# Performance work log

Measured on AMD Instinct MI355X. Metric: run time of the kernel, lower is better.

The kernel has to match this reference:

```python
import jax, jax.numpy as jnp
import numpy as np

D = 768      # input_dim
O = 768      # output_dim
E = 8        # num_experts
H = 10 * D   # expert hidden dim (fixed by module: input_dim * 10)
N = 4096     # tokens


def setup_inputs() -> dict:
    key = jax.random.key(0)
    ks = jax.random.split(key, 7)
    s = lambda fan_in: 1.0 / np.sqrt(fan_in)
    x  = jax.random.normal(ks[0], (N, D), dtype=jnp.float32)
    Wg = jax.random.uniform(ks[1], (D, E), jnp.float32, -s(D), s(D))
    bg = jax.random.uniform(ks[2], (E,),   jnp.float32, -s(D), s(D))
    W1 = jax.random.uniform(ks[3], (E, D, H), jnp.float32, -s(D), s(D))
    b1 = jax.random.uniform(ks[4], (E, H),    jnp.float32, -s(D), s(D))
    W2 = jax.random.uniform(ks[5], (E, H, O), jnp.float32, -s(H), s(H))
    b2 = jax.random.uniform(ks[6], (E, O),    jnp.float32, -s(H), s(H))
    return {"x": x, "Wg": Wg, "bg": bg, "W1": W1, "b1": b1, "W2": W2, "b2": b2}


def reference(x, Wg, bg, W1, b1, W2, b2):
    # gating: softmax over experts, keep only top-1 prob (rest zeroed)
    gate_probs = jax.nn.softmax(x @ Wg + bg, axis=1)          # [N, E]
    top_vals, top_idx = jax.lax.top_k(gate_probs, 1)           # [N, 1]
    gate_masked = jnp.zeros_like(gate_probs).at[
        jnp.arange(x.shape[0]), top_idx[:, 0]].set(top_vals[:, 0])
    # dense all-experts MLP (module computes every expert for every token)
    h = jax.nn.relu(jnp.einsum('nd,edh->neh', x, W1) + b1)     # [N, E, H]
    expert_out = jnp.einsum('neh,eho->neo', h, W2) + b2        # [N, E, O]
    # bmm combine: [N,1,E] @ [N,E,O] -> [N,O]
    return jnp.einsum('ne,neo->no', gate_masked, expert_out)
```

## Files before the change

### kernel.cpp

```cpp
#include <hip/hip_runtime.h>
#include <hip/hip_bf16.h>
#include <stdint.h>

#define N_TOK 4096
#define DIM   768
#define NE    8
#define HDIM  7680
#define ODIM  768
#define G1GRID 2816
#define G2GRID 1344

typedef __bf16 bf16x8 __attribute__((ext_vector_type(8)));
typedef float f32x4 __attribute__((ext_vector_type(4)));

__device__ __forceinline__ unsigned short f2bf(float f) {
    union { float f; unsigned u; } v; v.f = f;
    return (unsigned short)((v.u + 0x7fffu + ((v.u >> 16) & 1u)) >> 16);
}

__device__ __forceinline__ unsigned cvt_pk_bf16(float lo, float hi) {
    unsigned r;
    asm("v_cvt_pk_bf16_f32 %0, %1, %2" : "=v"(r) : "v"(lo), "v"(hi));
    return r;
}

__device__ __forceinline__ void gload_lds16(const unsigned short* g, unsigned short* l) {
    __builtin_amdgcn_global_load_lds(
        (const __attribute__((address_space(1))) unsigned int*)g,
        (__attribute__((address_space(3))) unsigned int*)l, 16, 0, 0);
}

__global__ void moe_gating(const float* __restrict__ x, const float* __restrict__ Wg,
                           const float* __restrict__ bg, int* __restrict__ cnt,
                           int* __restrict__ top_e, int* __restrict__ rnk,
                           float* __restrict__ top_p) {
    const int wid  = threadIdx.x >> 6;
    const int lane = threadIdx.x & 63;
    const int t = blockIdx.x * 4 + wid;
    double p[NE];
#pragma unroll
    for (int j = 0; j < NE; ++j) p[j] = 0.0;
    const float* xr  = x  + (size_t)t * DIM + lane * 12;
    const float* wr0 = Wg + lane * 12 * NE;
#pragma unroll
    for (int i = 0; i < 12; ++i) {
        double xv = (double)xr[i];
#pragma unroll
        for (int j = 0; j < NE; ++j) p[j] += xv * (double)wr0[i * NE + j];
    }
#pragma unroll
    for (int off = 32; off >= 1; off >>= 1)
#pragma unroll
        for (int j = 0; j < NE; ++j) p[j] += __shfl_xor(p[j], off, 64);
    if (lane == 0) {
        double l[NE];
#pragma unroll
        for (int j = 0; j < NE; ++j) l[j] = p[j] + (double)bg[j];
        int be = 0; double bl = l[0];
#pragma unroll
        for (int j = 1; j < NE; ++j) if (l[j] > bl) { bl = l[j]; be = j; }
        double s = 0.0;
#pragma unroll
        for (int j = 0; j < NE; ++j) s += exp(l[j] - bl);
        int rk = atomicAdd(&cnt[be], 1);
        top_e[t] = be; rnk[t] = rk; top_p[t] = (float)(1.0 / s);
    }
}

__global__ void moe_init(int* cnt) { if (threadIdx.x < NE) cnt[threadIdx.x] = 0; }

__global__ void moe_scan(const int* __restrict__ cnt, int* __restrict__ offs,
                         int* __restrict__ mc, int* __restrict__ g1s,
                         int* __restrict__ g2s) {
    __shared__ int smc[NE];
    int tid = threadIdx.x;
    if (tid == 0) { int s = 0; for (int e = 0; e < NE; ++e) { offs[e] = s; s += cnt[e]; } }
    if (tid < NE) { smc[tid] = (cnt[tid] + 127) >> 7; mc[tid] = smc[tid]; }
    __syncthreads();
    if (tid < 8) {
        int s = 0;
        for (int j = 0; j < 60; ++j) { int p = tid + 8 * j; g1s[p] = s; s += smc[p / 60]; }
        int s2 = 0;
        for (int j = 0; j < 6; ++j)  { int p = tid + 8 * j; g2s[p] = s2; s2 += 4 * smc[p / 6]; }
    }
}

__global__ void moe_fill(const int* __restrict__ mc, const int* __restrict__ g1s,
                         const int* __restrict__ g2s, int* __restrict__ tbl1,
                         int* __restrict__ tbl2) {
    int gid = blockIdx.x * 256 + threadIdx.x;
    if (gid < G1GRID) {
        int c = gid & 7, slot = gid >> 3;
        int sel = c;
        for (int j = 0; j < 60; ++j) { int p = c + 8 * j; if (g1s[p] <= slot) sel = p; else break; }
        int e = sel / 60, n0 = sel % 60;
        int mt = slot - g1s[sel];
        tbl1[gid] = (mt < mc[e]) ? ((e << 14) | (mt << 8) | (n0 << 2)) : -1;
    } else if (gid < G1GRID + G2GRID) {
        int gg = gid - G1GRID;
        int c = gg & 7, slot = gg >> 3;
        int sel = c;
        for (int j = 0; j < 6; ++j) { int p = c + 8 * j; if (g2s[p] <= slot) sel = p; else break; }
        int e = sel / 6, n0 = sel % 6;
        int mem = slot - g2s[sel];
        int mcE = mc[e];
        int ks = mem / mcE, mt = mem - ks * mcE;
        tbl2[gg] = (mem < 4 * mcE) ? ((e << 14) | (mt << 8) | (n0 << 2) | ks) : -1;
    }
}

__global__ void moe_mkperm(const int* __restrict__ top_e, const int* __restrict__ rnk,
                           const float* __restrict__ top_p, const int* __restrict__ offs,
                           int* __restrict__ perm, float* __restrict__ gate_s) {
    int t = blockIdx.x * 256 + threadIdx.x;
    int e = top_e[t];
    int slot = offs[e] + rnk[t];
    perm[slot] = t;
    gate_s[slot] = top_p[t];
}

__global__ void moe_gather(const float* __restrict__ x, const int* __restrict__ perm,
                           unsigned short* __restrict__ Xg) {
    int slot = blockIdx.x;
    int t = perm[slot];
    const float* src = x + (size_t)t * DIM;
    unsigned short* dst = Xg + (size_t)slot * DIM;
    for (int i = threadIdx.x; i < DIM; i += 256) dst[i] = f2bf(src[i]);
}

__global__ void moe_initout(const int* __restrict__ top_e, const float* __restrict__ top_p,
                            const float* __restrict__ b2, float* __restrict__ out) {
    int t = blockIdx.x;
    int e = top_e[t];
    float gv = top_p[t];
    const float* b = b2 + (size_t)e * ODIM;
    float* o = out + (size_t)t * ODIM;
    for (int i = threadIdx.x; i < ODIM; i += 256) o[i] = gv * b[i];
}

template<int LAYER>
__global__ __launch_bounds__(256, 3) void moe_gemm(
    const unsigned short* __restrict__ A, const float* __restrict__ B,
    const float* __restrict__ bias, const int* __restrict__ cnt,
    const int* __restrict__ offs, const int* __restrict__ perm,
    const float* __restrict__ gate_s, const int* __restrict__ tbl,
    unsigned short* __restrict__ H, float* __restrict__ out) {

    constexpr int NT    = (LAYER == 1) ? HDIM : ODIM;
    constexpr int AST   = (LAYER == 1) ? DIM  : HDIM;
    constexpr int KFULL = (LAYER == 1) ? DIM  : HDIM;
    constexpr int KBLK  = (LAYER == 1) ? DIM  : HDIM / 4;
    constexpr int NITER = KBLK / 32;

    const int code = tbl[blockIdx.x];
    if (code < 0) return;
    const int e  = code >> 14;
    const int mt = (code >> 8) & 63;
    const int n0 = ((code >> 2) & 63) * 128;
    const int ks = code & 3;
    const int ne = cnt[e];
    const int base = offs[e];
    const int mlim = ne - mt * 128;
    const int kbase = ks * KBLK;

    __shared__ __align__(16) unsigned short As[3][4096];
    __shared__ __align__(16) unsigned short Bs[2][4096];

    const int tid = threadIdx.x;
    const int lane = tid & 63, w = tid >> 6;
    const int wr = w >> 1, wc = w & 1;
    const int g = lane >> 4, r = lane & 15;

    const int rl0 = 2 * w * 16 + r;
    const int rl1 = rl0 + 16;
    const int cr0 = rl0 < mlim ? rl0 : mlim - 1;
    const int cr1 = rl1 < mlim ? rl1 : mlim - 1;
    const unsigned short* aS0 = A + (size_t)(base + mt * 128 + cr0) * AST + kbase + g * 8;
    const unsigned short* aS1 = A + (size_t)(base + mt * 128 + cr1) * AST + kbase + g * 8;
    const int aD0 = (2 * w) * 512;
    const int aD1 = aD0 + 512;

    const int bn = tid & 127;
    const int kh = tid >> 7;
    const float* bS = B + (size_t)e * KFULL * NT + (size_t)(kbase + kh * 16) * NT + n0 + bn;
    const int bD = (bn >> 4) * 512 + (kh * 2) * 128 + (bn & 15) * 8;

    f32x4 acc[4][4] = {};
    float bvA[16], bvB[16];

    unsigned short* A0 = &As[0][0];
    unsigned short* A1 = &As[1][0];
    unsigned short* A2 = &As[2][0];

#define LOADB(dst_, t_)                                                        \
    do { const float* bp_ = bS + (size_t)((t_) * 32) * NT;                     \
        _Pragma("unroll")                                                      \
        for (int i_ = 0; i_ < 16; ++i_) dst_[i_] = bp_[(size_t)i_ * NT];       \
    } while (0)

#define DMA_A(t_, abase_)                                                      \
    do { gload_lds16(aS0 + (t_) * 32, (abase_) + aD0);                         \
         gload_lds16(aS1 + (t_) * 32, (abase_) + aD1); } while (0)

#define COMMITB(src_, buf_)                                                    \
    do { uint4 q0_, q1_;                                                       \
        q0_.x = cvt_pk_bf16(src_[0],  src_[1]);  q0_.y = cvt_pk_bf16(src_[2],  src_[3]);  \
        q0_.z = cvt_pk_bf16(src_[4],  src_[5]);  q0_.w = cvt_pk_bf16(src_[6],  src_[7]);  \
        q1_.x = cvt_pk_bf16(src_[8],  src_[9]);  q1_.y = cvt_pk_bf16(src_[10], src_[11]); \
        q1_.z = cvt_pk_bf16(src_[12], src_[13]); q1_.w = cvt_pk_bf16(src_[14], src_[15]); \
        *(uint4*)&Bs[buf_][bD]       = q0_;                                    \
        *(uint4*)&Bs[buf_][bD + 128] = q1_;                                    \
    } while (0)

#define PHASE_END                                                              \
    do { asm volatile("s_waitcnt lgkmcnt(0)" ::: "memory");                    \
         __builtin_amdgcn_s_barrier();                                         \
         __builtin_amdgcn_sched_barrier(0); } while (0)

#define BODY(t_, cur_, ARD_, ADMA_, LDst_, CMsrc_, MODE_)                      \
    do {                                                                       \
        bf16x8 af_[4], bf_[4];                                                 \
        _Pragma("unroll")                                                      \
        for (int m_ = 0; m_ < 4; ++m_)                                         \
            af_[m_] = *(const bf16x8*)((ARD_) + (wr * 4 + m_) * 512 + lane * 8); \
        _Pragma("unroll")                                                      \
        for (int n_ = 0; n_ < 4; ++n_)                                         \
            bf_[n_] = *(const bf16x8*)&Bs[cur_][(wc * 4 + n_) * 512 + lane * 8]; \
        if (MODE_ == 2) DMA_A((t_) + 2, ADMA_);                                \
        if (MODE_ == 2) LOADB(LDst_, (t_) + 2);                                \
        _Pragma("unroll")                                                      \
        for (int n_ = 0; n_ < 4; ++n_)                                         \
            _Pragma("unroll")                                                  \
            for (int m_ = 0; m_ < 4; ++m_)                                     \
                acc[m_][n_] = __builtin_amdgcn_mfma_f32_16x16x32_bf16(         \
                    af_[m_], bf_[n_], acc[m_][n_], 0, 0, 0);                   \
        if (MODE_ >= 1) { COMMITB(CMsrc_, (cur_) ^ 1); PHASE_END; }            \
    } while (0)

    DMA_A(0, A0);
    LOADB(bvA, 0);
    DMA_A(1, A1);
    LOADB(bvB, 1);
    COMMITB(bvA, 0);
    PHASE_END;

#pragma unroll 1
    for (int t = 0; t + 4 <= NITER; t += 2) {
        BODY(t,     0, A0, A2, bvA, bvB, 2);
        BODY(t + 1, 1, A1, A0, bvB, bvA, 2);
        unsigned short* tr_ = A2; A2 = A1; A1 = A0; A0 = tr_;
    }
    BODY(NITER - 2, 0, A0, A2, bvA, bvB, 1);
    BODY(NITER - 1, 1, A1, A2, bvB, bvA, 0);

#undef BODY
#undef PHASE_END
#undef COMMITB
#undef DMA_A
#undef LOADB

#pragma unroll
    for (int m = 0; m < 4; ++m) {
#pragma unroll
        for (int j = 0; j < 4; ++j) {
            int lrow = mt * 128 + wr * 64 + m * 16 + g * 4 + j;
            if (lrow < ne) {
                int slot = base + lrow;
#pragma unroll
                for (int n = 0; n < 4; ++n) {
                    int col = n0 + wc * 64 + n * 16 + r;
                    if constexpr (LAYER == 1) {
                        float v = acc[m][n][j] + bias[(size_t)e * NT + col];
                        v = fmaxf(v, 0.0f);
                        H[(size_t)slot * HDIM + col] = f2bf(v);
                    } else {
                        atomicAdd(&out[(size_t)perm[slot] * ODIM + col],
                                  gate_s[slot] * acc[m][n][j]);
                    }
                }
            }
        }
    }
}

extern "C" void kernel_launch(void* const* d_in, const int* in_sizes, int n_in,
                              void* d_out, int out_size, void* d_ws, size_t ws_size,
                              hipStream_t stream) {
    const float* x  = (const float*)d_in[0];
    const float* Wg = (const float*)d_in[1];
    const float* bg = (const float*)d_in[2];
    const float* W1 = (const float*)d_in[3];
    const float* b1 = (const float*)d_in[4];
    const float* W2 = (const float*)d_in[5];
    const float* b2 = (const float*)d_in[6];
    float* out = (float*)d_out;

    char* ws = (char*)d_ws;
    int*   cnt    = (int*)(ws + 0);
    int*   offs   = (int*)(ws + 64);
    int*   mc     = (int*)(ws + 128);
    int*   g1s    = (int*)(ws + 256);
    int*   g2s    = (int*)(ws + 2304);
    int*   tbl1   = (int*)(ws + 3072);
    int*   tbl2   = (int*)(ws + 14336);
    int*   top_e  = (int*)(ws + 19712);
    int*   rnk    = (int*)(ws + 19712 + 16384);
    float* top_p  = (float*)(ws + 19712 + 2 * 16384);
    int*   perm   = (int*)(ws + 19712 + 3 * 16384);
    float* gate_s = (float*)(ws + 19712 + 4 * 16384);
    unsigned short* Xg = (unsigned short*)(ws + 101632);
    unsigned short* H  = (unsigned short*)(ws + 101632 + (size_t)N_TOK * DIM * 2);

    moe_init<<<1, 64, 0, stream>>>(cnt);
    moe_gating<<<N_TOK / 4, 256, 0, stream>>>(x, Wg, bg, cnt, top_e, rnk, top_p);
    moe_scan<<<1, 64, 0, stream>>>(cnt, offs, mc, g1s, g2s);
    moe_fill<<<(G1GRID + G2GRID + 255) / 256, 256, 0, stream>>>(mc, g1s, g2s, tbl1, tbl2);
    moe_mkperm<<<N_TOK / 256, 256, 0, stream>>>(top_e, rnk, top_p, offs, perm, gate_s);
    moe_gather<<<N_TOK, 256, 0, stream>>>(x, perm, Xg);
    moe_initout<<<N_TOK, 256, 0, stream>>>(top_e, top_p, b2, out);

    moe_gemm<1><<<G1GRID, 256, 0, stream>>>(Xg, W1, b1, cnt, offs, perm, gate_s, tbl1, H, out);
    moe_gemm<2><<<G2GRID, 256, 0, stream>>>(H, W2, b2, cnt, offs, perm, gate_s, tbl2, H, out);
}
```

Before: 369.0 us.

## Pre-transpose weights to bf16 and use 256-row, 512-thread GEMM tiles

Adds a transpose kernel that converts W1 and W2 from fp32 to bf16, K-major, on every call, so both operands can be streamed straight into LDS with global_load_lds. The grouped GEMM now uses 512-thread blocks with 256-row M tiles, a K step of 64 and a triple-buffered shared buffer. Tile count halves (smaller grid tables), and per-iteration register conversion of B is removed. In exchange, each call pays an extra pass that reads all weights in fp32 and writes them back in bf16, and occupancy drops to one block per CU.

New measurement: 459.1 us. 24.4% more time.

```diff
diff --git a/kernel.cpp b/kernel.cpp
--- a/kernel.cpp
+++ b/kernel.cpp
@@ -7,8 +7,8 @@
 #define NE    8
 #define HDIM  7680
 #define ODIM  768
-#define G1GRID 2816
-#define G2GRID 1344
+#define G1GRID 1536
+#define G2GRID 768
 
 typedef __bf16 bf16x8 __attribute__((ext_vector_type(8)));
 typedef float f32x4 __attribute__((ext_vector_type(4)));
@@ -16,12 +16,6 @@
 __device__ __forceinline__ unsigned short f2bf(float f) {
     union { float f; unsigned u; } v; v.f = f;
     return (unsigned short)((v.u + 0x7fffu + ((v.u >> 16) & 1u)) >> 16);
-}
-
-__device__ __forceinline__ unsigned cvt_pk_bf16(float lo, float hi) {
-    unsigned r;
-    asm("v_cvt_pk_bf16_f32 %0, %1, %2" : "=v"(r) : "v"(lo), "v"(hi));
-    return r;
 }
 
 __device__ __forceinline__ void gload_lds16(const unsigned short* g, unsigned short* l) {
@@ -75,7 +69,7 @@
     __shared__ int smc[NE];
     int tid = threadIdx.x;
     if (tid == 0) { int s = 0; for (int e = 0; e < NE; ++e) { offs[e] = s; s += cnt[e]; } }
-    if (tid < NE) { smc[tid] = (cnt[tid] + 127) >> 7; mc[tid] = smc[tid]; }
+    if (tid < NE) { smc[tid] = (cnt[tid] + 255) >> 8; mc[tid] = smc[tid]; }
     __syncthreads();
     if (tid < 8) {
         int s = 0;
@@ -138,9 +132,38 @@
     for (int i = threadIdx.x; i < ODIM; i += 256) o[i] = gv * b[i];
 }
 
+__global__ __launch_bounds__(256) void moe_wtrans(const float* __restrict__ in,
+                                                  unsigned short* __restrict__ outw,
+                                                  int K, int N) {
+    __shared__ __align__(16) unsigned short t[64][72];
+    const int tid = threadIdx.x;
+    const float* src = in + (size_t)blockIdx.z * K * N + (size_t)(blockIdx.y * 64) * N
+                          + blockIdx.x * 64;
+    unsigned short* dst = outw + (size_t)blockIdx.z * K * N + (size_t)(blockIdx.x * 64) * K
+                               + blockIdx.y * 64;
+    const int kr = tid >> 4;
+    const int nc = (tid & 15) * 4;
+#pragma unroll
+    for (int p = 0; p < 4; ++p) {
+        float4 v = *(const float4*)(src + (size_t)(p * 16 + kr) * N + nc);
+        t[nc + 0][p * 16 + kr] = f2bf(v.x);
+        t[nc + 1][p * 16 + kr] = f2bf(v.y);
+        t[nc + 2][p * 16 + kr] = f2bf(v.z);
+        t[nc + 3][p * 16 + kr] = f2bf(v.w);
+    }
+    __syncthreads();
+    const int nr = tid >> 3;
+    const int kc = (tid & 7) * 8;
+#pragma unroll
+    for (int p = 0; p < 2; ++p) {
+        uint4 q = *(const uint4*)&t[p * 32 + nr][kc];
+        *(uint4*)(dst + (size_t)(p * 32 + nr) * K + kc) = q;
+    }
+}
+
 template<int LAYER>
-__global__ __launch_bounds__(256, 3) void moe_gemm(
-    const unsigned short* __restrict__ A, const float* __restrict__ B,
+__global__ __launch_bounds__(512, 1) void moe_gemm8(
+    const unsigned short* __restrict__ A, const unsigned short* __restrict__ Wt,
     const float* __restrict__ bias, const int* __restrict__ cnt,
     const int* __restrict__ offs, const int* __restrict__ perm,
     const float* __restrict__ gate_s, const int* __restrict__ tbl,
@@ -150,7 +173,7 @@
     constexpr int AST   = (LAYER == 1) ? DIM  : HDIM;
     constexpr int KFULL = (LAYER == 1) ? DIM  : HDIM;
     constexpr int KBLK  = (LAYER == 1) ? DIM  : HDIM / 4;
-    constexpr int NITER = KBLK / 32;
+    constexpr int NITER = KBLK / 64;
 
     const int code = tbl[blockIdx.x];
     if (code < 0) return;
@@ -160,110 +183,85 @@
     const int ks = code & 3;
     const int ne = cnt[e];
     const int base = offs[e];
-    const int mlim = ne - mt * 128;
+    const int mlim = ne - mt * 256;
     const int kbase = ks * KBLK;
 
-    __shared__ __align__(16) unsigned short As[3][4096];
-    __shared__ __align__(16) unsigned short Bs[2][4096];
+    __shared__ __align__(16) unsigned short L[73728];
 
     const int tid = threadIdx.x;
     const int lane = tid & 63, w = tid >> 6;
     const int wr = w >> 1, wc = w & 1;
     const int g = lane >> 4, r = lane & 15;
 
-    const int rl0 = 2 * w * 16 + r;
-    const int rl1 = rl0 + 16;
-    const int cr0 = rl0 < mlim ? rl0 : mlim - 1;
-    const int cr1 = rl1 < mlim ? rl1 : mlim - 1;
-    const unsigned short* aS0 = A + (size_t)(base + mt * 128 + cr0) * AST + kbase + g * 8;
-    const unsigned short* aS1 = A + (size_t)(base + mt * 128 + cr1) * AST + kbase + g * 8;
-    const int aD0 = (2 * w) * 512;
-    const int aD1 = aD0 + 512;
-
-    const int bn = tid & 127;
-    const int kh = tid >> 7;
-    const float* bS = B + (size_t)e * KFULL * NT + (size_t)(kbase + kh * 16) * NT + n0 + bn;
-    const int bD = (bn >> 4) * 512 + (kh * 2) * 128 + (bn & 15) * 8;
+    const int rA0 = w * 32 + r, rA1 = rA0 + 16;
+    const int cA0 = rA0 < mlim ? rA0 : mlim - 1;
+    const int cA1 = rA1 < mlim ? rA1 : mlim - 1;
+    const unsigned short* aS0 = A + (size_t)(base + mt * 256 + cA0) * AST + kbase + g * 8;
+    const unsigned short* aS1 = A + (size_t)(base + mt * 256 + cA1) * AST + kbase + g * 8;
+    const unsigned short* bSp = Wt + (size_t)e * NT * KFULL
+                                + (size_t)(n0 + w * 16 + r) * KFULL + kbase + g * 8;
+    const int adc = w * 4;
+    const int bdc = w * 2;
 
     f32x4 acc[4][4] = {};
-    float bvA[16], bvB[16];
-
-    unsigned short* A0 = &As[0][0];
-    unsigned short* A1 = &As[1][0];
-    unsigned short* A2 = &As[2][0];
-
-#define LOADB(dst_, t_)                                                        \
-    do { const float* bp_ = bS + (size_t)((t_) * 32) * NT;                     \
-        _Pragma("unroll")                                                      \
-        for (int i_ = 0; i_ < 16; ++i_) dst_[i_] = bp_[(size_t)i_ * NT];       \
+
+#define STG(t2_, ssb_, kk_)                                                    \
+    do { int ko_ = (t2_) * 64 + (kk_) * 32;                                    \
+        gload_lds16(aS0 + ko_, &L[(ssb_) + (adc + 0 + (kk_)) * 512]);          \
+        gload_lds16(aS1 + ko_, &L[(ssb_) + (adc + 2 + (kk_)) * 512]);          \
+        gload_lds16(bSp + ko_, &L[(ssb_) + 16384 + (bdc + (kk_)) * 512]);      \
     } while (0)
 
-#define DMA_A(t_, abase_)                                                      \
-    do { gload_lds16(aS0 + (t_) * 32, (abase_) + aD0);                         \
-         gload_lds16(aS1 + (t_) * 32, (abase_) + aD1); } while (0)
-
-#define COMMITB(src_, buf_)                                                    \
-    do { uint4 q0_, q1_;                                                       \
-        q0_.x = cvt_pk_bf16(src_[0],  src_[1]);  q0_.y = cvt_pk_bf16(src_[2],  src_[3]);  \
-        q0_.z = cvt_pk_bf16(src_[4],  src_[5]);  q0_.w = cvt_pk_bf16(src_[6],  src_[7]);  \
-        q1_.x = cvt_pk_bf16(src_[8],  src_[9]);  q1_.y = cvt_pk_bf16(src_[10], src_[11]); \
-        q1_.z = cvt_pk_bf16(src_[12], src_[13]); q1_.w = cvt_pk_bf16(src_[14], src_[15]); \
-        *(uint4*)&Bs[buf_][bD]       = q0_;                                    \
-        *(uint4*)&Bs[buf_][bD + 128] = q1_;                                    \
-    } while (0)
-
-#define PHASE_END                                                              \
-    do { asm volatile("s_waitcnt lgkmcnt(0)" ::: "memory");                    \
-         __builtin_amdgcn_s_barrier();                                         \
-         __builtin_amdgcn_sched_barrier(0); } while (0)
-
-#define BODY(t_, cur_, ARD_, ADMA_, LDst_, CMsrc_, MODE_)                      \
+#define PHASE(rb_, kk_, doSTG_, t2_, ssb_, VM_, doBAR_)                        \
     do {                                                                       \
         bf16x8 af_[4], bf_[4];                                                 \
         _Pragma("unroll")                                                      \
         for (int m_ = 0; m_ < 4; ++m_)                                         \
-            af_[m_] = *(const bf16x8*)((ARD_) + (wr * 4 + m_) * 512 + lane * 8); \
+            af_[m_] = *(const bf16x8*)&L[(rb_) + ((wr * 4 + m_) * 2 + (kk_)) * 512 + lane * 8]; \
         _Pragma("unroll")                                                      \
         for (int n_ = 0; n_ < 4; ++n_)                                         \
-            bf_[n_] = *(const bf16x8*)&Bs[cur_][(wc * 4 + n_) * 512 + lane * 8]; \
-        if (MODE_ == 2) DMA_A((t_) + 2, ADMA_);                                \
-        if (MODE_ == 2) LOADB(LDst_, (t_) + 2);                                \
+            bf_[n_] = *(const bf16x8*)&L[(rb_) + 16384 + ((wc * 4 + n_) * 2 + (kk_)) * 512 + lane * 8]; \
+        if (doSTG_) STG(t2_, ssb_, kk_);                                       \
+        __builtin_amdgcn_s_barrier();                                          \
+        asm volatile("s_waitcnt lgkmcnt(0)" ::: "memory");                     \
+        __builtin_amdgcn_sched_barrier(0);                                     \
+        __builtin_amdgcn_s_setprio(1);                                         \
         _Pragma("unroll")                                                      \
         for (int n_ = 0; n_ < 4; ++n_)                                         \
             _Pragma("unroll")                                                  \
             for (int m_ = 0; m_ < 4; ++m_)                                     \
                 acc[m_][n_] = __builtin_amdgcn_mfma_f32_16x16x32_bf16(         \
                     af_[m_], bf_[n_], acc[m_][n_], 0, 0, 0);                   \
-        if (MODE_ >= 1) { COMMITB(CMsrc_, (cur_) ^ 1); PHASE_END; }            \
+        __builtin_amdgcn_s_setprio(0);                                         \
+        if ((VM_) == 1) asm volatile("s_waitcnt vmcnt(6)" ::: "memory");       \
+        else if ((VM_) == 2) asm volatile("s_waitcnt vmcnt(0)" ::: "memory");  \
+        if (doBAR_) __builtin_amdgcn_s_barrier();                              \
     } while (0)
 
-    DMA_A(0, A0);
-    LOADB(bvA, 0);
-    DMA_A(1, A1);
-    LOADB(bvB, 1);
-    COMMITB(bvA, 0);
-    PHASE_END;
-
+    STG(0, 0, 0); STG(0, 0, 1);
+    STG(1, 24576, 0); STG(1, 24576, 1);
+    asm volatile("s_waitcnt vmcnt(6)" ::: "memory");
+    __builtin_amdgcn_s_barrier();
+    __builtin_amdgcn_sched_barrier(0);
+
+    int b0 = 0, b1 = 24576, b2 = 49152;
 #pragma unroll 1
-    for (int t = 0; t + 4 <= NITER; t += 2) {
-        BODY(t,     0, A0, A2, bvA, bvB, 2);
-        BODY(t + 1, 1, A1, A0, bvB, bvA, 2);
-        unsigned short* tr_ = A2; A2 = A1; A1 = A0; A0 = tr_;
-    }
-    BODY(NITER - 2, 0, A0, A2, bvA, bvB, 1);
-    BODY(NITER - 1, 1, A1, A2, bvB, bvA, 0);
-
-#undef BODY
-#undef PHASE_END
-#undef COMMITB
-#undef DMA_A
-#undef LOADB
+    for (int t = 0; t < NITER; ++t) {
+        const bool stg = (t < NITER - 2);
+        PHASE(b0, 0, stg, t + 2, b2, 0, 1);
+        const int vm = stg ? 1 : ((t == NITER - 2) ? 2 : 0);
+        PHASE(b0, 1, stg, t + 2, b2, vm, (t < NITER - 1) ? 1 : 0);
+        int tmp = b0; b0 = b1; b1 = b2; b2 = tmp;
+    }
+
+#undef PHASE
+#undef STG
 
 #pragma unroll
     for (int m = 0; m < 4; ++m) {
 #pragma unroll
         for (int j = 0; j < 4; ++j) {
-            int lrow = mt * 128 + wr * 64 + m * 16 + g * 4 + j;
+            int lrow = mt * 256 + wr * 64 + m * 16 + g * 4 + j;
             if (lrow < ne) {
                 int slot = base + lrow;
 #pragma unroll
@@ -302,14 +300,16 @@
     int*   g1s    = (int*)(ws + 256);
     int*   g2s    = (int*)(ws + 2304);
     int*   tbl1   = (int*)(ws + 3072);
-    int*   tbl2   = (int*)(ws + 14336);
+    int*   tbl2   = (int*)(ws + 10240);
     int*   top_e  = (int*)(ws + 19712);
     int*   rnk    = (int*)(ws + 19712 + 16384);
     float* top_p  = (float*)(ws + 19712 + 2 * 16384);
     int*   perm   = (int*)(ws + 19712 + 3 * 16384);
     float* gate_s = (float*)(ws + 19712 + 4 * 16384);
-    unsigned short* Xg = (unsigned short*)(ws + 101632);
-    unsigned short* H  = (unsigned short*)(ws + 101632 + (size_t)N_TOK * DIM * 2);
+    unsigned short* Xg  = (unsigned short*)(ws + 101632);
+    unsigned short* H   = (unsigned short*)(ws + 101632 + (size_t)N_TOK * DIM * 2);
+    unsigned short* W1t = (unsigned short*)(ws + 69307648ull);
+    unsigned short* W2t = (unsigned short*)(ws + 163679488ull);
 
     moe_init<<<1, 64, 0, stream>>>(cnt);
     moe_gating<<<N_TOK / 4, 256, 0, stream>>>(x, Wg, bg, cnt, top_e, rnk, top_p);
@@ -319,6 +319,11 @@
     moe_gather<<<N_TOK, 256, 0, stream>>>(x, perm, Xg);
     moe_initout<<<N_TOK, 256, 0, stream>>>(top_e, top_p, b2, out);
 
-    moe_gemm<1><<<G1GRID, 256, 0, stream>>>(Xg, W1, b1, cnt, offs, perm, gate_s, tbl1, H, out);
-    moe_gemm<2><<<G2GRID, 256, 0, stream>>>(H, W2, b2, cnt, offs, perm, gate_s, tbl2, H, out);
-}
+    moe_wtrans<<<dim3(HDIM / 64, DIM / 64, NE), 256, 0, stream>>>(W1, W1t, DIM, HDIM);
+    moe_wtrans<<<dim3(ODIM / 64, HDIM / 64, NE), 256, 0, stream>>>(W2, W2t, HDIM, ODIM);
+
+    moe_gemm8<1><<<G1GRID, 512, 0, stream>>>(
+        Xg, W1t, b1, cnt, offs, perm, gate_s, tbl1, H, out);
+    moe_gemm8<2><<<G2GRID, 512, 0, stream>>>(
+        H, W2t, b2, cnt, offs, perm, gate_s, tbl2, H, out);
+}
```

## Store gathered activations and hidden in 16-row tiled layout with padded expert offsets

Applied to the files above, without the earlier changes.

Expert segment offsets are padded to multiples of 128 rows, and the gathered bf16 input plus the hidden activations are stored in a blocked layout: 16-row groups, each holding 8-element k-chunks. Each wavefront's async LDS DMA then reads one contiguous 1 KB span per load instead of 16 strided rows, and the row-clamping logic goes away. Gather now scatters each token directly into its padded slot using top_e/rnk/offs, with vectorized 16-byte stores. The cost is scattered 2-byte stores for hidden writes in the layer-1 epilogue and reads of uninitialized padding rows, which are masked only at output.

Measured after the change: 356.4 us. 1.04x faster.

```diff
diff --git a/kernel.cpp b/kernel.cpp
--- a/kernel.cpp
+++ b/kernel.cpp
@@ -9,6 +9,11 @@
 #define ODIM  768
 #define G1GRID 2816
 #define G2GRID 1344
+#define KC1 96
+#define KC2 960
+#define XB1 (KC1 * 128)
+#define XB2 (KC2 * 128)
+#define NSLOT 5120
 
 typedef __bf16 bf16x8 __attribute__((ext_vector_type(8)));
 typedef float f32x4 __attribute__((ext_vector_type(4)));
@@ -74,7 +79,10 @@
                          int* __restrict__ g2s) {
     __shared__ int smc[NE];
     int tid = threadIdx.x;
-    if (tid == 0) { int s = 0; for (int e = 0; e < NE; ++e) { offs[e] = s; s += cnt[e]; } }
+    if (tid == 0) {
+        int s = 0;
+        for (int e = 0; e < NE; ++e) { offs[e] = s; s += (cnt[e] + 127) & ~127; }
+    }
     if (tid < NE) { smc[tid] = (cnt[tid] + 127) >> 7; mc[tid] = smc[tid]; }
     __syncthreads();
     if (tid < 8) {
@@ -119,13 +127,19 @@
     gate_s[slot] = top_p[t];
 }
 
-__global__ void moe_gather(const float* __restrict__ x, const int* __restrict__ perm,
+__global__ void moe_gather(const float* __restrict__ x, const int* __restrict__ top_e,
+                           const int* __restrict__ rnk, const int* __restrict__ offs,
                            unsigned short* __restrict__ Xg) {
-    int slot = blockIdx.x;
-    int t = perm[slot];
-    const float* src = x + (size_t)t * DIM;
-    unsigned short* dst = Xg + (size_t)slot * DIM;
-    for (int i = threadIdx.x; i < DIM; i += 256) dst[i] = f2bf(src[i]);
+    int t = blockIdx.x;
+    int slot = offs[top_e[t]] + rnk[t];
+    int kc = threadIdx.x;
+    if (kc < KC1) {
+        const float* s8 = x + (size_t)t * DIM + kc * 8;
+        union { uint4 q; unsigned short u[8]; } v;
+#pragma unroll
+        for (int j = 0; j < 8; ++j) v.u[j] = f2bf(s8[j]);
+        *(uint4*)&Xg[(size_t)(slot >> 4) * XB1 + kc * 128 + (slot & 15) * 8] = v.q;
+    }
 }
 
 __global__ void moe_initout(const int* __restrict__ top_e, const float* __restrict__ top_p,
@@ -147,7 +161,7 @@
     unsigned short* __restrict__ H, float* __restrict__ out) {
 
     constexpr int NT    = (LAYER == 1) ? HDIM : ODIM;
-    constexpr int AST   = (LAYER == 1) ? DIM  : HDIM;
+    constexpr int ABLK  = (LAYER == 1) ? XB1  : XB2;
     constexpr int KFULL = (LAYER == 1) ? DIM  : HDIM;
     constexpr int KBLK  = (LAYER == 1) ? DIM  : HDIM / 4;
     constexpr int NITER = KBLK / 32;
@@ -160,7 +174,6 @@
     const int ks = code & 3;
     const int ne = cnt[e];
     const int base = offs[e];
-    const int mlim = ne - mt * 128;
     const int kbase = ks * KBLK;
 
     __shared__ __align__(16) unsigned short As[3][4096];
@@ -171,12 +184,10 @@
     const int wr = w >> 1, wc = w & 1;
     const int g = lane >> 4, r = lane & 15;
 
-    const int rl0 = 2 * w * 16 + r;
-    const int rl1 = rl0 + 16;
-    const int cr0 = rl0 < mlim ? rl0 : mlim - 1;
-    const int cr1 = rl1 < mlim ? rl1 : mlim - 1;
-    const unsigned short* aS0 = A + (size_t)(base + mt * 128 + cr0) * AST + kbase + g * 8;
-    const unsigned short* aS1 = A + (size_t)(base + mt * 128 + cr1) * AST + kbase + g * 8;
+    const int ab16 = (base + mt * 128) >> 4;
+    const unsigned short* aS0 = A + (size_t)(ab16 + 2 * w) * ABLK
+                                  + (size_t)(kbase >> 3) * 128 + lane * 8;
+    const unsigned short* aS1 = aS0 + ABLK;
     const int aD0 = (2 * w) * 512;
     const int aD1 = aD0 + 512;
 
@@ -199,8 +210,8 @@
     } while (0)
 
 #define DMA_A(t_, abase_)                                                      \
-    do { gload_lds16(aS0 + (t_) * 32, (abase_) + aD0);                         \
-         gload_lds16(aS1 + (t_) * 32, (abase_) + aD1); } while (0)
+    do { gload_lds16(aS0 + (t_) * 512, (abase_) + aD0);                        \
+         gload_lds16(aS1 + (t_) * 512, (abase_) + aD1); } while (0)
 
 #define COMMITB(src_, buf_)                                                    \
     do { uint4 q0_, q1_;                                                       \
@@ -272,7 +283,8 @@
                     if constexpr (LAYER == 1) {
                         float v = acc[m][n][j] + bias[(size_t)e * NT + col];
                         v = fmaxf(v, 0.0f);
-                        H[(size_t)slot * HDIM + col] = f2bf(v);
+                        H[(size_t)(slot >> 4) * XB2 + (size_t)(col >> 3) * 128
+                          + (slot & 15) * 8 + (col & 7)] = f2bf(v);
                     } else {
                         atomicAdd(&out[(size_t)perm[slot] * ODIM + col],
                                   gate_s[slot] * acc[m][n][j]);
@@ -306,17 +318,17 @@
     int*   top_e  = (int*)(ws + 19712);
     int*   rnk    = (int*)(ws + 19712 + 16384);
     float* top_p  = (float*)(ws + 19712 + 2 * 16384);
-    int*   perm   = (int*)(ws + 19712 + 3 * 16384);
-    float* gate_s = (float*)(ws + 19712 + 4 * 16384);
-    unsigned short* Xg = (unsigned short*)(ws + 101632);
-    unsigned short* H  = (unsigned short*)(ws + 101632 + (size_t)N_TOK * DIM * 2);
+    int*   perm   = (int*)(ws + 68864);
+    float* gate_s = (float*)(ws + 89344);
+    unsigned short* Xg = (unsigned short*)(ws + 110592);
+    unsigned short* H  = (unsigned short*)(ws + 110592 + 320ull * XB1 * 2);
 
     moe_init<<<1, 64, 0, stream>>>(cnt);
     moe_gating<<<N_TOK / 4, 256, 0, stream>>>(x, Wg, bg, cnt, top_e, rnk, top_p);
     moe_scan<<<1, 64, 0, stream>>>(cnt, offs, mc, g1s, g2s);
     moe_fill<<<(G1GRID + G2GRID + 255) / 256, 256, 0, stream>>>(mc, g1s, g2s, tbl1, tbl2);
     moe_mkperm<<<N_TOK / 256, 256, 0, stream>>>(top_e, rnk, top_p, offs, perm, gate_s);
-    moe_gather<<<N_TOK, 256, 0, stream>>>(x, perm, Xg);
+    moe_gather<<<N_TOK, 128, 0, stream>>>(x, top_e, rnk, offs, Xg);
     moe_initout<<<N_TOK, 256, 0, stream>>>(top_e, top_p, b2, out);
 
     moe_gemm<1><<<G1GRID, 256, 0, stream>>>(Xg, W1, b1, cnt, offs, perm, gate_s, tbl1, H, out);
```
